# Kernel tuning notes

Hardware: AMD Instinct MI355X
Metric: run time of the kernel (lower is better)

Reference implementation:

```python
import jax, jax.numpy as jnp
import numpy as np

TEMPERATURE = 8.0  # sqrt(d_k) with d_k = 64

def setup_inputs() -> dict:
    key = jax.random.key(0)
    kq, kk, kv = jax.random.split(key, 3)
    B, L, D = 16, 2048, 64  # heads, seq_len, head_dim
    q = jax.random.normal(kq, (B, L, D), dtype=jnp.float32)
    k = jax.random.normal(kk, (B, L, D), dtype=jnp.float32)
    v = jax.random.normal(kv, (B, L, D), dtype=jnp.float32)
    return {"q": q, "k": k, "v": v}

def reference(q, k, v):
    # scores: [B, Lq, Lk]
    scores = jnp.einsum('bqd,bkd->bqk', q, k) / TEMPERATURE
    log_attn = jax.nn.log_softmax(scores, axis=-1)
    attn = jnp.exp(log_attn)  # softmax, reusing the single stable reduction
    out = jnp.einsum('bqk,bkd->bqd', attn, v)        # [B, Lq, Dv]
    B, Lk, Dv = v.shape
    # transpose(0,1).reshape(Lk, Dv*B): heads folded into feature dim
    output = jnp.transpose(out, (1, 0, 2)).reshape(Lk, Dv * B)
    return (output, attn, log_attn)
```

## Files before the change

### kernel.cpp

```cpp
#include <hip/hip_runtime.h>

#define LSEQ 2048
#define NH   16
#define HD   64

typedef __attribute__((ext_vector_type(8))) short short8;
typedef __attribute__((ext_vector_type(4))) float f32x4;

__device__ __forceinline__ unsigned short f2b(float x) {
  unsigned int u = __builtin_bit_cast(unsigned int, x);
  u += 0x7FFFu + ((u >> 16) & 1u);
  return (unsigned short)(u >> 16);
}

__global__ __launch_bounds__(256) void prep_kernel(
    const float* __restrict__ q, const float* __restrict__ k, const float* __restrict__ v,
    unsigned short* __restrict__ qb, unsigned short* __restrict__ kb,
    unsigned short* __restrict__ vt) {
  const int b = blockIdx.y, lt = blockIdx.x;
  const int t = threadIdx.x;
  __shared__ float vlds[64][65];
  const int l0 = lt * 64;
  #pragma unroll
  for (int i = 0; i < 4; ++i) {
    int r = (t >> 4) + 16 * i;
    size_t base = ((size_t)(b * LSEQ + l0 + r)) * HD + (t & 15) * 4;
    float4 qv = *(const float4*)(q + base);
    float4 kv = *(const float4*)(k + base);
    float4 vv = *(const float4*)(v + base);
    ushort4 qo, ko;
    qo.x = f2b(qv.x * 0.125f); qo.y = f2b(qv.y * 0.125f);
    qo.z = f2b(qv.z * 0.125f); qo.w = f2b(qv.w * 0.125f);
    ko.x = f2b(kv.x); ko.y = f2b(kv.y); ko.z = f2b(kv.z); ko.w = f2b(kv.w);
    *(ushort4*)(qb + base) = qo;
    *(ushort4*)(kb + base) = ko;
    int c = (t & 15) * 4;
    vlds[r][c] = vv.x; vlds[r][c + 1] = vv.y; vlds[r][c + 2] = vv.z; vlds[r][c + 3] = vv.w;
  }
  __syncthreads();
  const int ll = t & 63;
  const int dbase = (t >> 6) * 16;
  #pragma unroll
  for (int i = 0; i < 16; ++i) {
    int d = dbase + i;
    vt[((size_t)(b * HD + d)) * LSEQ + l0 + ll] = f2b(vlds[ll][d]);
  }
}

__global__ __launch_bounds__(256) void attn_kernel(
    const unsigned short* __restrict__ qb, const unsigned short* __restrict__ kb,
    const unsigned short* __restrict__ vt,
    float* __restrict__ out0, float* __restrict__ attn, float* __restrict__ logp) {
  const int b = blockIdx.y, qt = blockIdx.x;
  const int t = threadIdx.x;
  const int w = t >> 6, lane = t & 63, quad = lane >> 4, l16 = lane & 15;
  __shared__ unsigned short ps[4][16][72];

  const int q0 = qt * 64;
  const int qrl = quad * 4;

  const unsigned short* qrow = qb + ((size_t)(b * LSEQ + q0 + w * 16 + l16)) * HD;
  short8 aq0 = *(const short8*)(qrow + quad * 8);
  short8 aq1 = *(const short8*)(qrow + 32 + quad * 8);

  float p0 = 0.f, p1 = 0.f, p2 = 0.f, p3 = 0.f;
  for (int kt = 0; kt < 32; ++kt) {
    const unsigned short* kbase = kb + ((size_t)(b * LSEQ + kt * 64)) * HD;
    #pragma unroll
    for (int nt = 0; nt < 4; ++nt) {
      const unsigned short* krow = kbase + (nt * 16 + l16) * HD + quad * 8;
      short8 b0 = *(const short8*)(krow);
      short8 b1 = *(const short8*)(krow + 32);
      f32x4 s = {0.f, 0.f, 0.f, 0.f};
      s = __builtin_amdgcn_mfma_f32_16x16x32_bf16(aq0, b0, s, 0, 0, 0);
      s = __builtin_amdgcn_mfma_f32_16x16x32_bf16(aq1, b1, s, 0, 0, 0);
      p0 += __expf(s[0]); p1 += __expf(s[1]);
      p2 += __expf(s[2]); p3 += __expf(s[3]);
    }
  }
  #pragma unroll
  for (int off = 1; off < 16; off <<= 1) {
    p0 += __shfl_xor(p0, off, 64);
    p1 += __shfl_xor(p1, off, 64);
    p2 += __shfl_xor(p2, off, 64);
    p3 += __shfl_xor(p3, off, 64);
  }
  const float logl0 = __logf(p0), logl1 = __logf(p1);
  const float logl2 = __logf(p2), logl3 = __logf(p3);

  f32x4 oacc[4] = {{0.f,0.f,0.f,0.f},{0.f,0.f,0.f,0.f},{0.f,0.f,0.f,0.f},{0.f,0.f,0.f,0.f}};
  const size_t arow0 = ((size_t)(b * LSEQ + q0 + w * 16 + qrl)) * LSEQ;

  for (int kt = 0; kt < 32; ++kt) {
    const unsigned short* kbase = kb + ((size_t)(b * LSEQ + kt * 64)) * HD;
    #pragma unroll
    for (int nt = 0; nt < 4; ++nt) {
      const unsigned short* krow = kbase + (nt * 16 + l16) * HD + quad * 8;
      short8 b0 = *(const short8*)(krow);
      short8 b1 = *(const short8*)(krow + 32);
      f32x4 s = {0.f, 0.f, 0.f, 0.f};
      s = __builtin_amdgcn_mfma_f32_16x16x32_bf16(aq0, b0, s, 0, 0, 0);
      s = __builtin_amdgcn_mfma_f32_16x16x32_bf16(aq1, b1, s, 0, 0, 0);
      const int col = kt * 64 + nt * 16 + l16;
      const float la0 = s[0] - logl0; const float a0 = __expf(la0);
      const float la1 = s[1] - logl1; const float a1 = __expf(la1);
      const float la2 = s[2] - logl2; const float a2 = __expf(la2);
      const float la3 = s[3] - logl3; const float a3 = __expf(la3);
      attn[arow0 + col]            = a0;  logp[arow0 + col]            = la0;
      attn[arow0 + LSEQ + col]     = a1;  logp[arow0 + LSEQ + col]     = la1;
      attn[arow0 + 2 * LSEQ + col] = a2;  logp[arow0 + 2 * LSEQ + col] = la2;
      attn[arow0 + 3 * LSEQ + col] = a3;  logp[arow0 + 3 * LSEQ + col] = la3;
      ps[w][qrl + 0][nt * 16 + l16] = f2b(a0);
      ps[w][qrl + 1][nt * 16 + l16] = f2b(a1);
      ps[w][qrl + 2][nt * 16 + l16] = f2b(a2);
      ps[w][qrl + 3][nt * 16 + l16] = f2b(a3);
    }
    asm volatile("s_waitcnt lgkmcnt(0)" ::: "memory");
    short8 ap0 = *(const short8*)(&ps[w][l16][quad * 8]);
    short8 ap1 = *(const short8*)(&ps[w][l16][32 + quad * 8]);
    #pragma unroll
    for (int nt = 0; nt < 4; ++nt) {
      const unsigned short* vrow =
          vt + ((size_t)(b * HD + nt * 16 + l16)) * LSEQ + kt * 64 + quad * 8;
      short8 v0 = *(const short8*)(vrow);
      short8 v1 = *(const short8*)(vrow + 32);
      oacc[nt] = __builtin_amdgcn_mfma_f32_16x16x32_bf16(ap0, v0, oacc[nt], 0, 0, 0);
      oacc[nt] = __builtin_amdgcn_mfma_f32_16x16x32_bf16(ap1, v1, oacc[nt], 0, 0, 0);
    }
    asm volatile("s_waitcnt lgkmcnt(0)" ::: "memory");
  }

  #pragma unroll
  for (int nt = 0; nt < 4; ++nt) {
    #pragma unroll
    for (int r = 0; r < 4; ++r) {
      out0[((size_t)(q0 + w * 16 + qrl + r)) * (NH * HD) + b * HD + nt * 16 + l16] =
          oacc[nt][r];
    }
  }
}

extern "C" void kernel_launch(void* const* d_in, const int* in_sizes, int n_in,
                              void* d_out, int out_size, void* d_ws, size_t ws_size,
                              hipStream_t stream) {
  const float* q = (const float*)d_in[0];
  const float* k = (const float*)d_in[1];
  const float* v = (const float*)d_in[2];
  float* out0 = (float*)d_out;
  float* attn = out0 + (size_t)LSEQ * NH * HD;
  float* logp = attn + (size_t)NH * LSEQ * LSEQ;

  unsigned short* qb = (unsigned short*)d_ws;
  unsigned short* kb = qb + (size_t)NH * LSEQ * HD;
  unsigned short* vt = kb + (size_t)NH * LSEQ * HD;

  dim3 grid(LSEQ / 64, NH);
  prep_kernel<<<grid, 256, 0, stream>>>(q, k, v, qb, kb, vt);
  attn_kernel<<<grid, 256, 0, stream>>>(qb, kb, vt, out0, attn, logp);
}
```

Measured before the change: 701.0 us.

## Split key range across blocks, transpose S tile, vectorize attn stores, XCD-aware mapping

Computes S^T so each lane owns one query row with four contiguous key columns. This turns the attn and logp writes into 16-byte vector stores and lets P be repacked into the MFMA operand by lane shuffles instead of going through LDS. The grid doubles: each block handles half the key range for the output phase, with partial outputs combined by atomicAdd into an output buffer zeroed by a memset. Blocks are remapped so each XCD serves two heads for L2 locality. The cost is that the full row-sum pass now runs twice per query tile, plus extra atomics and a memset.

Result: slower. 779.8 us (+11.2%).

```diff
diff --git a/kernel.cpp b/kernel.cpp
--- a/kernel.cpp
+++ b/kernel.cpp
@@ -6,11 +6,15 @@
 
 typedef __attribute__((ext_vector_type(8))) short short8;
 typedef __attribute__((ext_vector_type(4))) float f32x4;
+typedef __attribute__((ext_vector_type(4))) unsigned int uint4v;
 
 __device__ __forceinline__ unsigned short f2b(float x) {
   unsigned int u = __builtin_bit_cast(unsigned int, x);
   u += 0x7FFFu + ((u >> 16) & 1u);
   return (unsigned short)(u >> 16);
+}
+__device__ __forceinline__ unsigned int pack2(float lo, float hi) {
+  return (unsigned int)f2b(lo) | ((unsigned int)f2b(hi) << 16);
 }
 
 __global__ __launch_bounds__(256) void prep_kernel(
@@ -47,96 +51,108 @@
   }
 }
 
-__global__ __launch_bounds__(256) void attn_kernel(
+__global__ __launch_bounds__(256, 4) void attn_kernel(
     const unsigned short* __restrict__ qb, const unsigned short* __restrict__ kb,
     const unsigned short* __restrict__ vt,
     float* __restrict__ out0, float* __restrict__ attn, float* __restrict__ logp) {
-  const int b = blockIdx.y, qt = blockIdx.x;
+  const int lid  = blockIdx.x;
+  const int xcd  = lid & 7;
+  const int jj   = lid >> 3;
+  const int b    = xcd * 2 + (jj & 1);
+  const int rest = jj >> 1;
+  const int qt   = rest & 31;
+  const int half = rest >> 5;
+
   const int t = threadIdx.x;
   const int w = t >> 6, lane = t & 63, quad = lane >> 4, l16 = lane & 15;
-  __shared__ unsigned short ps[4][16][72];
 
-  const int q0 = qt * 64;
-  const int qrl = quad * 4;
+  const int qrow = qt * 64 + w * 16 + l16;
 
-  const unsigned short* qrow = qb + ((size_t)(b * LSEQ + q0 + w * 16 + l16)) * HD;
-  short8 aq0 = *(const short8*)(qrow + quad * 8);
-  short8 aq1 = *(const short8*)(qrow + 32 + quad * 8);
+  const unsigned short* qp = qb + ((size_t)(b * LSEQ + qrow)) * HD + quad * 8;
+  short8 bq0 = *(const short8*)(qp);
+  short8 bq1 = *(const short8*)(qp + 32);
 
-  float p0 = 0.f, p1 = 0.f, p2 = 0.f, p3 = 0.f;
-  for (int kt = 0; kt < 32; ++kt) {
-    const unsigned short* kbase = kb + ((size_t)(b * LSEQ + kt * 64)) * HD;
+  const unsigned short* kbh = kb + (size_t)b * LSEQ * HD;
+  const unsigned short* vth = vt + (size_t)b * HD * LSEQ;
+
+  float psum = 0.f;
+  for (int kc = 0; kc < LSEQ; kc += 32) {
+    const unsigned short* k0 = kbh + (size_t)(kc + l16) * HD + quad * 8;
+    const unsigned short* k1 = k0 + 16 * HD;
+    short8 ka00 = *(const short8*)(k0);
+    short8 ka01 = *(const short8*)(k0 + 32);
+    short8 ka10 = *(const short8*)(k1);
+    short8 ka11 = *(const short8*)(k1 + 32);
+    f32x4 s0 = {0.f, 0.f, 0.f, 0.f}, s1 = {0.f, 0.f, 0.f, 0.f};
+    s0 = __builtin_amdgcn_mfma_f32_16x16x32_bf16(ka00, bq0, s0, 0, 0, 0);
+    s0 = __builtin_amdgcn_mfma_f32_16x16x32_bf16(ka01, bq1, s0, 0, 0, 0);
+    s1 = __builtin_amdgcn_mfma_f32_16x16x32_bf16(ka10, bq0, s1, 0, 0, 0);
+    s1 = __builtin_amdgcn_mfma_f32_16x16x32_bf16(ka11, bq1, s1, 0, 0, 0);
+    psum += __expf(s0[0]) + __expf(s0[1]) + __expf(s0[2]) + __expf(s0[3]);
+    psum += __expf(s1[0]) + __expf(s1[1]) + __expf(s1[2]) + __expf(s1[3]);
+  }
+  psum += __shfl_xor(psum, 16, 64);
+  psum += __shfl_xor(psum, 32, 64);
+  const float logl = __logf(psum);
+
+  f32x4 oacc[4] = {{0.f,0.f,0.f,0.f},{0.f,0.f,0.f,0.f},{0.f,0.f,0.f,0.f},{0.f,0.f,0.f,0.f}};
+  float* attn_r = attn + ((size_t)(b * LSEQ + qrow)) * LSEQ;
+  float* logp_r = logp + ((size_t)(b * LSEQ + qrow)) * LSEQ;
+
+  const int kcs = half * (LSEQ / 2);
+  for (int kc = kcs; kc < kcs + LSEQ / 2; kc += 32) {
+    const unsigned short* k0 = kbh + (size_t)(kc + l16) * HD + quad * 8;
+    const unsigned short* k1 = k0 + 16 * HD;
+    short8 ka00 = *(const short8*)(k0);
+    short8 ka01 = *(const short8*)(k0 + 32);
+    short8 ka10 = *(const short8*)(k1);
+    short8 ka11 = *(const short8*)(k1 + 32);
+    f32x4 s0 = {0.f, 0.f, 0.f, 0.f}, s1 = {0.f, 0.f, 0.f, 0.f};
+    s0 = __builtin_amdgcn_mfma_f32_16x16x32_bf16(ka00, bq0, s0, 0, 0, 0);
+    s0 = __builtin_amdgcn_mfma_f32_16x16x32_bf16(ka01, bq1, s0, 0, 0, 0);
+    s1 = __builtin_amdgcn_mfma_f32_16x16x32_bf16(ka10, bq0, s1, 0, 0, 0);
+    s1 = __builtin_amdgcn_mfma_f32_16x16x32_bf16(ka11, bq1, s1, 0, 0, 0);
+
+    f32x4 la0 = s0 - logl, la1 = s1 - logl;
+    f32x4 a0, a1;
+    a0[0] = __expf(la0[0]); a0[1] = __expf(la0[1]);
+    a0[2] = __expf(la0[2]); a0[3] = __expf(la0[3]);
+    a1[0] = __expf(la1[0]); a1[1] = __expf(la1[1]);
+    a1[2] = __expf(la1[2]); a1[3] = __expf(la1[3]);
+    *(f32x4*)(attn_r + kc + quad * 4)      = a0;
+    *(f32x4*)(logp_r + kc + quad * 4)      = la0;
+    *(f32x4*)(attn_r + kc + 16 + quad * 4) = a1;
+    *(f32x4*)(logp_r + kc + 16 + quad * 4) = la1;
+
+    unsigned int p00 = pack2(a0[0], a0[1]);
+    unsigned int p01 = pack2(a0[2], a0[3]);
+    unsigned int p10 = pack2(a1[0], a1[1]);
+    unsigned int p11 = pack2(a1[2], a1[3]);
+    uint4v bfv;
     #pragma unroll
-    for (int nt = 0; nt < 4; ++nt) {
-      const unsigned short* krow = kbase + (nt * 16 + l16) * HD + quad * 8;
-      short8 b0 = *(const short8*)(krow);
-      short8 b1 = *(const short8*)(krow + 32);
-      f32x4 s = {0.f, 0.f, 0.f, 0.f};
-      s = __builtin_amdgcn_mfma_f32_16x16x32_bf16(aq0, b0, s, 0, 0, 0);
-      s = __builtin_amdgcn_mfma_f32_16x16x32_bf16(aq1, b1, s, 0, 0, 0);
-      p0 += __expf(s[0]); p1 += __expf(s[1]);
-      p2 += __expf(s[2]); p3 += __expf(s[3]);
+    for (int d = 0; d < 4; ++d) {
+      int srcl = ((lane & 16) << 1) + ((d >> 1) << 4) + l16;
+      unsigned int v0 = __shfl((d & 1) ? p01 : p00, srcl, 64);
+      unsigned int v1 = __shfl((d & 1) ? p11 : p10, srcl, 64);
+      bfv[d] = (lane & 32) ? v1 : v0;
+    }
+    short8 bp = __builtin_bit_cast(short8, bfv);
+
+    #pragma unroll
+    for (int db = 0; db < 4; ++db) {
+      const unsigned short* vp = vth + (size_t)(db * 16 + l16) * LSEQ + kc + quad * 8;
+      short8 va = *(const short8*)(vp);
+      oacc[db] = __builtin_amdgcn_mfma_f32_16x16x32_bf16(va, bp, oacc[db], 0, 0, 0);
     }
   }
+
+  float* op = out0 + (size_t)qrow * (NH * HD) + b * HD + quad * 4;
   #pragma unroll
-  for (int off = 1; off < 16; off <<= 1) {
-    p0 += __shfl_xor(p0, off, 64);
-    p1 += __shfl_xor(p1, off, 64);
-    p2 += __shfl_xor(p2, off, 64);
-    p3 += __shfl_xor(p3, off, 64);
-  }
-  const float logl0 = __logf(p0), logl1 = __logf(p1);
-  const float logl2 = __logf(p2), logl3 = __logf(p3);
-
-  f32x4 oacc[4] = {{0.f,0.f,0.f,0.f},{0.f,0.f,0.f,0.f},{0.f,0.f,0.f,0.f},{0.f,0.f,0.f,0.f}};
-  const size_t arow0 = ((size_t)(b * LSEQ + q0 + w * 16 + qrl)) * LSEQ;
-
-  for (int kt = 0; kt < 32; ++kt) {
-    const unsigned short* kbase = kb + ((size_t)(b * LSEQ + kt * 64)) * HD;
-    #pragma unroll
-    for (int nt = 0; nt < 4; ++nt) {
-      const unsigned short* krow = kbase + (nt * 16 + l16) * HD + quad * 8;
-      short8 b0 = *(const short8*)(krow);
-      short8 b1 = *(const short8*)(krow + 32);
-      f32x4 s = {0.f, 0.f, 0.f, 0.f};
-      s = __builtin_amdgcn_mfma_f32_16x16x32_bf16(aq0, b0, s, 0, 0, 0);
-      s = __builtin_amdgcn_mfma_f32_16x16x32_bf16(aq1, b1, s, 0, 0, 0);
-      const int col = kt * 64 + nt * 16 + l16;
-      const float la0 = s[0] - logl0; const float a0 = __expf(la0);
-      const float la1 = s[1] - logl1; const float a1 = __expf(la1);
-      const float la2 = s[2] - logl2; const float a2 = __expf(la2);
-      const float la3 = s[3] - logl3; const float a3 = __expf(la3);
-      attn[arow0 + col]            = a0;  logp[arow0 + col]            = la0;
-      attn[arow0 + LSEQ + col]     = a1;  logp[arow0 + LSEQ + col]     = la1;
-      attn[arow0 + 2 * LSEQ + col] = a2;  logp[arow0 + 2 * LSEQ + col] = la2;
-      attn[arow0 + 3 * LSEQ + col] = a3;  logp[arow0 + 3 * LSEQ + col] = la3;
-      ps[w][qrl + 0][nt * 16 + l16] = f2b(a0);
-      ps[w][qrl + 1][nt * 16 + l16] = f2b(a1);
-      ps[w][qrl + 2][nt * 16 + l16] = f2b(a2);
-      ps[w][qrl + 3][nt * 16 + l16] = f2b(a3);
-    }
-    asm volatile("s_waitcnt lgkmcnt(0)" ::: "memory");
-    short8 ap0 = *(const short8*)(&ps[w][l16][quad * 8]);
-    short8 ap1 = *(const short8*)(&ps[w][l16][32 + quad * 8]);
-    #pragma unroll
-    for (int nt = 0; nt < 4; ++nt) {
-      const unsigned short* vrow =
-          vt + ((size_t)(b * HD + nt * 16 + l16)) * LSEQ + kt * 64 + quad * 8;
-      short8 v0 = *(const short8*)(vrow);
-      short8 v1 = *(const short8*)(vrow + 32);
-      oacc[nt] = __builtin_amdgcn_mfma_f32_16x16x32_bf16(ap0, v0, oacc[nt], 0, 0, 0);
-      oacc[nt] = __builtin_amdgcn_mfma_f32_16x16x32_bf16(ap1, v1, oacc[nt], 0, 0, 0);
-    }
-    asm volatile("s_waitcnt lgkmcnt(0)" ::: "memory");
-  }
-
-  #pragma unroll
-  for (int nt = 0; nt < 4; ++nt) {
-    #pragma unroll
-    for (int r = 0; r < 4; ++r) {
-      out0[((size_t)(q0 + w * 16 + qrl + r)) * (NH * HD) + b * HD + nt * 16 + l16] =
-          oacc[nt][r];
-    }
+  for (int db = 0; db < 4; ++db) {
+    atomicAdd(op + db * 16 + 0, oacc[db][0]);
+    atomicAdd(op + db * 16 + 1, oacc[db][1]);
+    atomicAdd(op + db * 16 + 2, oacc[db][2]);
+    atomicAdd(op + db * 16 + 3, oacc[db][3]);
   }
 }
 
@@ -154,7 +170,9 @@
   unsigned short* kb = qb + (size_t)NH * LSEQ * HD;
   unsigned short* vt = kb + (size_t)NH * LSEQ * HD;
 
-  dim3 grid(LSEQ / 64, NH);
-  prep_kernel<<<grid, 256, 0, stream>>>(q, k, v, qb, kb, vt);
-  attn_kernel<<<grid, 256, 0, stream>>>(qb, kb, vt, out0, attn, logp);
+  hipMemsetAsync(out0, 0, (size_t)LSEQ * NH * HD * sizeof(float), stream);
+
+  dim3 pgrid(LSEQ / 64, NH);
+  prep_kernel<<<pgrid, 256, 0, stream>>>(q, k, v, qb, kb, vt);
+  attn_kernel<<<1024, 256, 0, stream>>>(qb, kb, vt, out0, attn, logp);
 }
```
